# Optimization experiments

Measured on AMD Instinct MI355X. Metric: run time of the kernel, lower is better.

The kernel has to match this reference:

```python
import jax, jax.numpy as jnp
import numpy as np

EPS = 1e-8

def _normalize(a):
    return a / jnp.clip(jnp.linalg.norm(a, axis=-1, keepdims=True), EPS)

def _cosine(a, b):
    # pairwise cosine similarity: [Na, d] x [Nb, d] -> [Na, Nb]
    return _normalize(a) @ _normalize(b).T

def setup_inputs() -> dict:
    key = jax.random.key(0)
    n, k, q, d = 100, 5, 75, 4096
    x = jax.random.normal(key, (n * (k + q), d), dtype=jnp.float32)
    tao = jnp.full((1,), 10.0, dtype=jnp.float32)
    return {"x": x, "tao": tao, "n": n, "k": k, "q": q}

def reference(x, tao, n, k, q):
    d = x.shape[-1]
    x = x.reshape(n, k + q, d)
    support = x[:, :k]                      # [n, k, d]
    query = x[:, k:].reshape(n * q, d)      # [NQ, d]
    NQ = n * q
    proto = support.mean(axis=1)            # [n, d]

    pre_sim = _cosine(query, proto)         # [NQ, n]
    pre_label = jnp.argmax(pre_sim, axis=1) # [NQ]

    # vectorized per-class masked softmax aggregation (replaces Python loop)
    cls_ids = jnp.arange(n)
    mask = pre_label[None, :] == cls_ids[:, None]            # [n, NQ]
    logits_q = jnp.where(mask, pre_sim.T, -jnp.inf)          # [n, NQ]
    proto_n = _normalize(proto)
    self_sim = jnp.sum(proto_n * proto_n, axis=-1)           # [n], cosine(proto, proto)
    logits = jnp.concatenate([logits_q, self_sim[:, None]], axis=1)  # [n, NQ+1]
    w = jax.nn.softmax(logits, axis=1)                       # [n, NQ+1]
    adapted_proto = w[:, :NQ] @ query + w[:, NQ:] * proto    # [n, d]

    sim = _cosine(query, adapted_proto)                      # [NQ, n]
    return tao.reshape(()) * sim
```

## Files before the change

### kernel.cpp

```cpp
#include <hip/hip_runtime.h>
#include <hip/hip_bf16.h>
#include <math.h>

#define NQUERY 7500
#define NCLS   100
#define DIM    4096
#define KQ     75
#define KSUP   5
#define RPC    80
#define MPAD   7552
#define NPAD   112
#define CAPQ   256
#define RCAP   2048
#define EPSF   1e-8f
#define SELEM  845824
#define SLICE_BYTES 3383296u

typedef __attribute__((ext_vector_type(8))) short bf16x8;
typedef __attribute__((ext_vector_type(4))) float f32x4;

__device__ __forceinline__ int xrow_of_query(int j) {
    return (j / KQ) * RPC + KSUP + (j % KQ);
}
__device__ __forceinline__ short bf16t(float x) {
    union { float f; unsigned u; } v; v.f = x;
    return (short)(v.u >> 16);
}
__device__ __forceinline__ float bf16hi(float x) {
    union { float f; unsigned u; } v; v.f = x;
    v.u &= 0xFFFF0000u; return v.f;
}
__device__ __forceinline__ void gload_lds16(const short* g, short* l) {
    __builtin_amdgcn_global_load_lds(
        (const __attribute__((address_space(1))) unsigned int*)g,
        (__attribute__((address_space(3))) unsigned int*)l, 16, 0, 0);
}

__global__ __launch_bounds__(256) void k_proto1(const float* __restrict__ x,
        float* __restrict__ proto, float* __restrict__ norm2) {
    const int c = blockIdx.x, ch = blockIdx.y, t = threadIdx.x;
    const int i = ch * 1024 + t * 4;
    const float* b0 = x + (size_t)(c * RPC) * DIM;
    f32x4 s = {0.f, 0.f, 0.f, 0.f};
#pragma unroll
    for (int r = 0; r < KSUP; ++r)
        s += *(const f32x4*)(b0 + (size_t)r * DIM + i);
    s = s / 5.0f;
    *(f32x4*)(proto + (size_t)c*DIM + i) = s;
    float ssq = s[0]*s[0] + s[1]*s[1] + s[2]*s[2] + s[3]*s[3];
    for (int o = 32; o; o >>= 1) ssq += __shfl_down(ssq, o);
    if ((t & 63) == 0) atomicAdd(&norm2[c], ssq);
}

__global__ __launch_bounds__(256) void k_proto2(const float* __restrict__ proto,
        const float* __restrict__ norm2, short* __restrict__ Phi, short* __restrict__ Plo,
        float* __restrict__ es) {
    const int c = blockIdx.x, t = threadIdx.x;
    const int nt = c >> 4, lm = c & 15;
    if (c >= NCLS) {
        for (int g = t; g < 512; g += 256) {
            const int kstep = g >> 2, kq = g & 3;
            size_t o = (((size_t)(nt * 128 + kstep) * 4 + kq) * 16 + lm) * 8;
            bf16x8 z = {0,0,0,0,0,0,0,0};
            *(bf16x8*)(Phi + o) = z;
            *(bf16x8*)(Plo + o) = z;
        }
        return;
    }
    const float tot = norm2[c];
    const float inv = 1.f / fmaxf(sqrtf(tot), EPSF);
    if (t == 0) es[c] = expf(tot * inv * inv);
    for (int g = t; g < 512; g += 256) {
        const int kstep = g >> 2, kq = g & 3;
        const float* src = proto + (size_t)c * DIM + kstep * 32 + kq * 8;
        f32x4 a = *(const f32x4*)src, b = *(const f32x4*)(src + 4);
        float fv[8] = {a[0],a[1],a[2],a[3],b[0],b[1],b[2],b[3]};
        bf16x8 h, l;
#pragma unroll
        for (int e = 0; e < 8; ++e) {
            float pn = fv[e] * inv;
            float hh = bf16hi(pn);
            h[e] = bf16t(pn);
            l[e] = bf16t(pn - hh);
        }
        size_t o = (((size_t)(nt * 128 + kstep) * 4 + kq) * 16 + lm) * 8;
        *(bf16x8*)(Phi + o) = h;
        *(bf16x8*)(Plo + o) = l;
    }
}

template<int TNKS>
__global__ __launch_bounds__(256) void k_gemm1(const float* __restrict__ x,
        const short* __restrict__ Phi, const short* __restrict__ Plo,
        float* __restrict__ Spart, float* __restrict__ nq2) {
    constexpr int KST = 128 / TNKS;
    constexpr int NG  = KST / 2;
    __shared__ short bbuf[28 * 512];
    const int bx = blockIdx.x, kz = blockIdx.y;
    const int w = threadIdx.x >> 6, lane = threadIdx.x & 63;
    const int lm = lane & 15, kq = lane >> 4;
    const int mt = bx * 4 + w;
    const int j = mt * 16 + lm;
    const int jc = j < NQUERY ? j : NQUERY - 1;
    const float* pa = x + (size_t)xrow_of_query(jc) * DIM + kq * 8;
    const int ks0 = kz * KST;

    f32x4 acc[7];
#pragma unroll
    for (int nt = 0; nt < 7; ++nt) acc[nt] = (f32x4){0.f,0.f,0.f,0.f};
    float ssq = 0.f;

    for (int g = 0; g < NG; ++g) {
        const int gk = ks0 + g * 2;
#pragma unroll
        for (int p = 0; p < 7; ++p) {
            const int cid = w * 7 + p;
            const int s = cid / 14, r = cid % 14, nt = r >> 1, hl = r & 1;
            const short* gsrc = (hl ? Plo : Phi) + ((size_t)(nt * 128 + gk + s) << 9);
            gload_lds16(gsrc + lane * 8, &bbuf[(cid << 9) + lane * 8]);
        }
        __syncthreads();
#pragma unroll
        for (int s = 0; s < 2; ++s) {
            const float* pas = pa + (gk + s) * 32;
            f32x4 f0 = *(const f32x4*)(pas);
            f32x4 f1 = *(const f32x4*)(pas + 4);
            float fv[8] = {f0[0],f0[1],f0[2],f0[3],f1[0],f1[1],f1[2],f1[3]};
            bf16x8 ah, al;
#pragma unroll
            for (int e = 0; e < 8; ++e) {
                float xx = fv[e];
                ssq += xx * xx;
                float hh = bf16hi(xx);
                ah[e] = bf16t(xx);
                al[e] = bf16t(xx - hh);
            }
#pragma unroll
            for (int nt = 0; nt < 7; ++nt) {
                const bf16x8 bh = *(const bf16x8*)(&bbuf[((s*14 + nt*2 + 0) << 9) + lane * 8]);
                const bf16x8 bl = *(const bf16x8*)(&bbuf[((s*14 + nt*2 + 1) << 9) + lane * 8]);
                acc[nt] = __builtin_amdgcn_mfma_f32_16x16x32_bf16(ah, bh, acc[nt], 0, 0, 0);
                acc[nt] = __builtin_amdgcn_mfma_f32_16x16x32_bf16(ah, bl, acc[nt], 0, 0, 0);
                acc[nt] = __builtin_amdgcn_mfma_f32_16x16x32_bf16(al, bh, acc[nt], 0, 0, 0);
            }
        }
        __syncthreads();
    }
    float s2 = ssq;
    s2 += __shfl_xor(s2, 16);
    s2 += __shfl_xor(s2, 32);
    if (kq == 0 && j < NQUERY) atomicAdd(&nq2[j], s2);

    float* sp = Spart + (size_t)kz * SELEM + (size_t)(mt * 16) * NPAD;
#pragma unroll
    for (int nt = 0; nt < 7; ++nt)
#pragma unroll
        for (int r = 0; r < 4; ++r)
            sp[(size_t)(kq * 4 + r) * NPAD + nt * 16 + lm] = acc[nt][r];
}

__global__ __launch_bounds__(256) void k_reduce1(const float* __restrict__ Spart,
        float* __restrict__ Sred, int nks) {
    const int idx = blockIdx.x * 256 + threadIdx.x;
    const size_t e = (size_t)idx * 4;
    f32x4 s = {0.f, 0.f, 0.f, 0.f};
    for (int kz = 0; kz < nks; ++kz)
        s += *(const f32x4*)(Spart + (size_t)kz * SELEM + e);
    *(f32x4*)(Sred + e) = s;
}

__global__ __launch_bounds__(256) void k_argmax(const float* __restrict__ S,
        const float* __restrict__ nq2, int* __restrict__ label, float* __restrict__ coef,
        float* __restrict__ invq, int* __restrict__ rcnt, int* __restrict__ rlist) {
    const int j = blockIdx.x * 256 + threadIdx.x;
    if (j >= NQUERY) return;
    const float* row = S + (size_t)j * NPAD;
    float m1 = -1e30f, m2 = -1e30f;
    int i1 = 0, i2 = 0;
    for (int c = 0; c < NCLS; ++c) {
        float v = row[c];
        if (v > m1) { m2 = m1; i2 = i1; m1 = v; i1 = c; }
        else if (v > m2) { m2 = v; i2 = c; }
    }
    const float inv = 1.f / fmaxf(sqrtf(nq2[j]), EPSF);
    invq[j] = inv;
    label[j] = i1;
    coef[j] = expf(m1 * inv);
    if ((m1 - m2) * inv < 1e-4f) {
        int p = atomicAdd(rcnt, 1);
        if (p < RCAP) rlist[p] = j | (i1 << 13) | (i2 << 20);
    }
}

__global__ __launch_bounds__(64) void k_refine(const float* __restrict__ x,
        const float* __restrict__ S, const float* __restrict__ invq,
        int* __restrict__ label, float* __restrict__ coef,
        const int* __restrict__ rcnt, const int* __restrict__ rlist) {
    const int cnt = min(*rcnt, RCAP);
    const int lane = threadIdx.x;
    for (int e = blockIdx.x; e < cnt; e += gridDim.x) {
        const int pk = rlist[e];
        const int j = pk & 8191, c1 = (pk >> 13) & 127, c2 = (pk >> 20) & 127;
        const float* xq = x + (size_t)xrow_of_query(j) * DIM;
        const int cc[2] = {c1, c2};
        double cosv[2];
#pragma unroll
        for (int s = 0; s < 2; ++s) {
            const float* xb = x + (size_t)(cc[s] * RPC) * DIM;
            double dt = 0.0, pp = 0.0, q2 = 0.0;
            for (int i = lane; i < DIM; i += 64) {
                double p = (double)xb[i] + (double)xb[i + DIM] + (double)xb[i + 2*DIM]
                         + (double)xb[i + 3*DIM] + (double)xb[i + 4*DIM];
                double qv = (double)xq[i];
                dt += p * qv; pp += p * p; q2 += qv * qv;
            }
            for (int o = 32; o; o >>= 1) {
                dt += __shfl_down(dt, o);
                pp += __shfl_down(pp, o);
                q2 += __shfl_down(q2, o);
            }
            cosv[s] = dt / (sqrt(pp) * sqrt(q2));
        }
        if (lane == 0) {
            int win = (cosv[1] > cosv[0] || (cosv[1] == cosv[0] && c2 < c1)) ? c2 : c1;
            if (win != c1) {
                label[j] = win;
                coef[j] = expf(S[(size_t)j * NPAD + win] * invq[j]);
            }
        }
    }
}

__global__ __launch_bounds__(256) void k_lists(const int* __restrict__ label,
        int* __restrict__ cls_cnt, int* __restrict__ cls_list) {
    const int j = blockIdx.x * 256 + threadIdx.x;
    if (j >= NQUERY) return;
    const int c = label[j];
    const int p = atomicAdd(&cls_cnt[c], 1);
    if (p < CAPQ) cls_list[c * CAPQ + p] = j;
}

__global__ __launch_bounds__(128) void k_adapt(const float* __restrict__ x,
        const float* __restrict__ coef, const int* __restrict__ cls_cnt,
        const int* __restrict__ cls_list, float* __restrict__ APpart) {
    const int cx = blockIdx.x, c = blockIdx.y, sl = blockIdx.z;
    const int i0 = cx * 512 + threadIdx.x * 4;
    const int n = min(cls_cnt[c], CAPQ);
    f32x4 acc = {0.f, 0.f, 0.f, 0.f};
    for (int e = sl; e < n; e += 4) {
        const int j = cls_list[c * CAPQ + e];
        const float cf = coef[j];
        const f32x4 v = *(const f32x4*)(x + (size_t)xrow_of_query(j) * DIM + i0);
        acc += v * cf;
    }
    *(f32x4*)(APpart + (size_t)sl * NCLS * DIM + (size_t)c * DIM + i0) = acc;
}

__global__ __launch_bounds__(256) void k_ap1(float* __restrict__ APpart,
        const float* __restrict__ proto, const float* __restrict__ es,
        float* __restrict__ norm2b) {
    const int c = blockIdx.x, ch = blockIdx.y, t = threadIdx.x;
    const int i = ch * 1024 + t * 4;
    const float e = es[c];
    f32x4 s = {0.f, 0.f, 0.f, 0.f};
#pragma unroll
    for (int sl = 0; sl < 4; ++sl)
        s += *(const f32x4*)(APpart + (size_t)sl * NCLS * DIM + (size_t)c * DIM + i);
    f32x4 pr = *(const f32x4*)(proto + (size_t)c*DIM + i);
    s += pr * e;
    *(f32x4*)(APpart + (size_t)c*DIM + i) = s;
    float ssq = s[0]*s[0] + s[1]*s[1] + s[2]*s[2] + s[3]*s[3];
    for (int o = 32; o; o >>= 1) ssq += __shfl_down(ssq, o);
    if ((t & 63) == 0) atomicAdd(&norm2b[c], ssq);
}

__global__ __launch_bounds__(256) void k_ap2(const float* __restrict__ AP0,
        const float* __restrict__ norm2b, short* __restrict__ APhi) {
    const int c = blockIdx.x, t = threadIdx.x;
    const int nt = c >> 4, lm = c & 15;
    if (c >= NCLS) {
        for (int g = t; g < 512; g += 256) {
            const int kstep = g >> 2, kq = g & 3;
            size_t o = (((size_t)(nt * 128 + kstep) * 4 + kq) * 16 + lm) * 8;
            bf16x8 z = {0,0,0,0,0,0,0,0};
            *(bf16x8*)(APhi + o) = z;
        }
        return;
    }
    const float inv = 1.f / fmaxf(sqrtf(norm2b[c]), EPSF);
    for (int g = t; g < 512; g += 256) {
        const int kstep = g >> 2, kq = g & 3;
        const float* src = AP0 + (size_t)c * DIM + kstep * 32 + kq * 8;
        f32x4 a = *(const f32x4*)src, b = *(const f32x4*)(src + 4);
        float fv[8] = {a[0],a[1],a[2],a[3],b[0],b[1],b[2],b[3]};
        bf16x8 h;
#pragma unroll
        for (int e = 0; e < 8; ++e) h[e] = bf16t(fv[e] * inv);
        size_t o = (((size_t)(nt * 128 + kstep) * 4 + kq) * 16 + lm) * 8;
        *(bf16x8*)(APhi + o) = h;
    }
}

template<int TNKS>
__global__ __launch_bounds__(256) void k_gemm2(const float* __restrict__ x,
        const short* __restrict__ APhi, float* __restrict__ Opart) {
    constexpr int KST = 128 / TNKS;
    constexpr int NG  = KST / 2;
    __shared__ short bbuf[14 * 512];
    const int bx = blockIdx.x, kz = blockIdx.y;
    const int w = threadIdx.x >> 6, lane = threadIdx.x & 63;
    const int lm = lane & 15, kq = lane >> 4;
    const int mt = bx * 4 + w;
    const int j = mt * 16 + lm;
    const int jc = j < NQUERY ? j : NQUERY - 1;
    const float* pa = x + (size_t)xrow_of_query(jc) * DIM + kq * 8;
    const int ks0 = kz * KST;

    f32x4 acc[7];
#pragma unroll
    for (int nt = 0; nt < 7; ++nt) acc[nt] = (f32x4){0.f,0.f,0.f,0.f};

    for (int g = 0; g < NG; ++g) {
        const int gk = ks0 + g * 2;
#pragma unroll
        for (int p = 0; p < 4; ++p) {
            const int cid = w * 4 + p;
            if (cid < 14) {
                const int s = cid / 7, nt = cid % 7;
                const short* gsrc = APhi + ((size_t)(nt * 128 + gk + s) << 9);
                gload_lds16(gsrc + lane * 8, &bbuf[(cid << 9) + lane * 8]);
            }
        }
        __syncthreads();
#pragma unroll
        for (int s = 0; s < 2; ++s) {
            const float* pas = pa + (gk + s) * 32;
            f32x4 f0 = *(const f32x4*)(pas);
            f32x4 f1 = *(const f32x4*)(pas + 4);
            float fv[8] = {f0[0],f0[1],f0[2],f0[3],f1[0],f1[1],f1[2],f1[3]};
            bf16x8 ah;
#pragma unroll
            for (int e = 0; e < 8; ++e) ah[e] = bf16t(fv[e]);
#pragma unroll
            for (int nt = 0; nt < 7; ++nt) {
                const bf16x8 bh = *(const bf16x8*)(&bbuf[((s*7 + nt) << 9) + lane * 8]);
                acc[nt] = __builtin_amdgcn_mfma_f32_16x16x32_bf16(ah, bh, acc[nt], 0, 0, 0);
            }
        }
        __syncthreads();
    }
    float* op = Opart + (size_t)kz * SELEM + (size_t)(mt * 16) * NPAD;
#pragma unroll
    for (int nt = 0; nt < 7; ++nt)
#pragma unroll
        for (int r = 0; r < 4; ++r)
            op[(size_t)(kq * 4 + r) * NPAD + nt * 16 + lm] = acc[nt][r];
}

__global__ __launch_bounds__(256) void k_reduce2(const float* __restrict__ Opart,
        const float* __restrict__ invq, const float* __restrict__ tao,
        float* __restrict__ out, int nks) {
    const int idx = blockIdx.x * 256 + threadIdx.x;
    if (idx >= NQUERY * 25) return;
    const int j = idx / 25, c4 = (idx % 25) * 4;
    const size_t e = (size_t)j * NPAD + c4;
    f32x4 s = {0.f, 0.f, 0.f, 0.f};
    for (int kz = 0; kz < nks; ++kz)
        s += *(const f32x4*)(Opart + (size_t)kz * SELEM + e);
    const float sc = tao[0] * invq[j];
    *(f32x4*)(out + (size_t)j * NCLS + c4) = s * sc;
}

#define OFF_RCNT   0u
#define OFF_CCNT   256u
#define OFF_N2     768u
#define OFF_N2B    1280u
#define OFF_NQ2    1792u
#define ZERO_BYTES 32768u
#define OFF_ES     32768u
#define OFF_INVQ   33280u
#define OFF_LABEL  63488u
#define OFF_COEF   93696u
#define OFF_RLIST  123904u
#define OFF_CLIST  132096u
#define OFF_PROTO  234496u
#define OFF_PHI    1872896u
#define OFF_PLO    2790400u
#define OFF_APHI   3707904u
#define OFF_SRED   4625408u
#define OFF_APPART 8008704u
#define OFF_PART   14562304u

extern "C" void kernel_launch(void* const* d_in, const int* in_sizes, int n_in,
                              void* d_out, int out_size, void* d_ws, size_t ws_size,
                              hipStream_t stream) {
    const float* x   = (const float*)d_in[0];
    const float* tao = (const float*)d_in[1];
    char* ws = (char*)d_ws;

    int*   rcnt    = (int*)  (ws + OFF_RCNT);
    int*   ccnt    = (int*)  (ws + OFF_CCNT);
    float* norm2   = (float*)(ws + OFF_N2);
    float* norm2b  = (float*)(ws + OFF_N2B);
    float* nq2     = (float*)(ws + OFF_NQ2);
    float* es      = (float*)(ws + OFF_ES);
    float* invq    = (float*)(ws + OFF_INVQ);
    int*   label   = (int*)  (ws + OFF_LABEL);
    float* coef    = (float*)(ws + OFF_COEF);
    int*   rlist   = (int*)  (ws + OFF_RLIST);
    int*   clist   = (int*)  (ws + OFF_CLIST);
    float* proto   = (float*)(ws + OFF_PROTO);
    short* Phi     = (short*)(ws + OFF_PHI);
    short* Plo     = (short*)(ws + OFF_PLO);
    short* APhi    = (short*)(ws + OFF_APHI);
    float* Sred    = (float*)(ws + OFF_SRED);
    float* APpart  = (float*)(ws + OFF_APPART);
    float* Part    = (float*)(ws + OFF_PART);

    int nks = 1;
    if (ws_size > (size_t)OFF_PART + SLICE_BYTES) {
        size_t avail = (ws_size - OFF_PART) / SLICE_BYTES;
        nks = avail >= 8 ? 8 : (int)avail;
        while (nks & (nks - 1)) nks &= nks - 1;
    }

    hipMemsetAsync(ws, 0, ZERO_BYTES, stream);

    k_proto1 <<<dim3(NCLS, 4), 256, 0, stream>>>(x, proto, norm2);
    k_proto2 <<<NPAD, 256, 0, stream>>>(proto, norm2, Phi, Plo, es);

    switch (nks) {
        case 8:  k_gemm1<8> <<<dim3(118, 8), 256, 0, stream>>>(x, Phi, Plo, Part, nq2); break;
        case 4:  k_gemm1<4> <<<dim3(118, 4), 256, 0, stream>>>(x, Phi, Plo, Part, nq2); break;
        case 2:  k_gemm1<2> <<<dim3(118, 2), 256, 0, stream>>>(x, Phi, Plo, Part, nq2); break;
        default: k_gemm1<1> <<<dim3(118, 1), 256, 0, stream>>>(x, Phi, Plo, Part, nq2); break;
    }
    k_reduce1<<<826, 256, 0, stream>>>(Part, Sred, nks);
    k_argmax <<<30, 256, 0, stream>>>(Sred, nq2, label, coef, invq, rcnt, rlist);
    k_refine <<<512, 64, 0, stream>>>(x, Sred, invq, label, coef, rcnt, rlist);
    k_lists  <<<30, 256, 0, stream>>>(label, ccnt, clist);
    k_adapt  <<<dim3(8, NCLS, 4), 128, 0, stream>>>(x, coef, ccnt, clist, APpart);
    k_ap1    <<<dim3(NCLS, 4), 256, 0, stream>>>(APpart, proto, es, norm2b);
    k_ap2    <<<NPAD, 256, 0, stream>>>(APpart, norm2b, APhi);
    switch (nks) {
        case 8:  k_gemm2<8> <<<dim3(118, 8), 256, 0, stream>>>(x, APhi, Part); break;
        case 4:  k_gemm2<4> <<<dim3(118, 4), 256, 0, stream>>>(x, APhi, Part); break;
        case 2:  k_gemm2<2> <<<dim3(118, 2), 256, 0, stream>>>(x, APhi, Part); break;
        default: k_gemm2<1> <<<dim3(118, 1), 256, 0, stream>>>(x, APhi, Part); break;
    }
    k_reduce2<<<733, 256, 0, stream>>>(Part, invq, tao, (float*)d_out, nks);
}
```

Baseline: 360.5 us.

## Fuse prototype and adapted-prototype norm kernels; allow 16-way K split

Merges k_proto1/k_proto2 into one kernel per class that computes the mean, the norm via a block reduction, and the bf16 hi/lo tiles. It also merges k_ap1/k_ap2 into k_apnorm the same way, which removes two launches and the global atomics. The K-split cap for both GEMMs rises from 8 to 16 when workspace allows, giving more blocks in flight at the cost of more partial sums to reduce. The fused kernels use only 100 blocks, so each one has more serial work.

```diff
diff --git a/kernel.cpp b/kernel.cpp
--- a/kernel.cpp
+++ b/kernel.cpp
@@ -17,6 +17,7 @@
 #define SLICE_BYTES 3383296u
 
 typedef __attribute__((ext_vector_type(8))) short bf16x8;
+typedef __attribute__((ext_vector_type(4))) short s16x4;
 typedef __attribute__((ext_vector_type(4))) float f32x4;
 
 __device__ __forceinline__ int xrow_of_query(int j) {
@@ -36,24 +37,12 @@
         (__attribute__((address_space(3))) unsigned int*)l, 16, 0, 0);
 }
 
-__global__ __launch_bounds__(256) void k_proto1(const float* __restrict__ x,
-        float* __restrict__ proto, float* __restrict__ norm2) {
-    const int c = blockIdx.x, ch = blockIdx.y, t = threadIdx.x;
-    const int i = ch * 1024 + t * 4;
-    const float* b0 = x + (size_t)(c * RPC) * DIM;
-    f32x4 s = {0.f, 0.f, 0.f, 0.f};
-#pragma unroll
-    for (int r = 0; r < KSUP; ++r)
-        s += *(const f32x4*)(b0 + (size_t)r * DIM + i);
-    s = s / 5.0f;
-    *(f32x4*)(proto + (size_t)c*DIM + i) = s;
-    float ssq = s[0]*s[0] + s[1]*s[1] + s[2]*s[2] + s[3]*s[3];
-    for (int o = 32; o; o >>= 1) ssq += __shfl_down(ssq, o);
-    if ((t & 63) == 0) atomicAdd(&norm2[c], ssq);
-}
-
-__global__ __launch_bounds__(256) void k_proto2(const float* __restrict__ proto,
-        const float* __restrict__ norm2, short* __restrict__ Phi, short* __restrict__ Plo,
+__device__ __forceinline__ size_t tile_off(int nt, int lm, int i) {
+    return (((size_t)(nt * 128 + (i >> 5)) * 4 + ((i >> 3) & 3)) * 16 + lm) * 8 + (i & 7);
+}
+
+__global__ __launch_bounds__(256) void k_proto(const float* __restrict__ x,
+        float* __restrict__ proto, short* __restrict__ Phi, short* __restrict__ Plo,
         float* __restrict__ es) {
     const int c = blockIdx.x, t = threadIdx.x;
     const int nt = c >> 4, lm = c & 15;
@@ -65,27 +54,51 @@
             *(bf16x8*)(Phi + o) = z;
             *(bf16x8*)(Plo + o) = z;
         }
+        if (t == 0) es[c] = 0.f;
         return;
     }
-    const float tot = norm2[c];
-    const float inv = 1.f / fmaxf(sqrtf(tot), EPSF);
-    if (t == 0) es[c] = expf(tot * inv * inv);
-    for (int g = t; g < 512; g += 256) {
-        const int kstep = g >> 2, kq = g & 3;
-        const float* src = proto + (size_t)c * DIM + kstep * 32 + kq * 8;
-        f32x4 a = *(const f32x4*)src, b = *(const f32x4*)(src + 4);
-        float fv[8] = {a[0],a[1],a[2],a[3],b[0],b[1],b[2],b[3]};
-        bf16x8 h, l;
-#pragma unroll
-        for (int e = 0; e < 8; ++e) {
-            float pn = fv[e] * inv;
+    __shared__ float red[4];
+    __shared__ float s_inv;
+    const float* b0 = x + (size_t)(c * RPC) * DIM;
+    float v[16];
+    float ssq = 0.f;
+#pragma unroll
+    for (int p = 0; p < 4; ++p) {
+        const int i = p * 1024 + t * 4;
+        f32x4 s = {0.f, 0.f, 0.f, 0.f};
+#pragma unroll
+        for (int r = 0; r < KSUP; ++r)
+            s += *(const f32x4*)(b0 + (size_t)r * DIM + i);
+        s = s / 5.0f;
+        *(f32x4*)&v[p*4] = s;
+        *(f32x4*)(proto + (size_t)c*DIM + i) = s;
+        ssq += s[0]*s[0] + s[1]*s[1] + s[2]*s[2] + s[3]*s[3];
+    }
+    for (int o = 32; o; o >>= 1) ssq += __shfl_down(ssq, o);
+    if ((t & 63) == 0) red[t >> 6] = ssq;
+    __syncthreads();
+    if (t == 0) {
+        float tot = red[0] + red[1] + red[2] + red[3];
+        float inv = 1.f / fmaxf(sqrtf(tot), EPSF);
+        s_inv = inv;
+        es[c] = expf(tot * inv * inv);
+    }
+    __syncthreads();
+    const float inv = s_inv;
+#pragma unroll
+    for (int p = 0; p < 4; ++p) {
+        const int i = p * 1024 + t * 4;
+        s16x4 h, l;
+#pragma unroll
+        for (int e = 0; e < 4; ++e) {
+            float pn = v[p*4+e] * inv;
             float hh = bf16hi(pn);
             h[e] = bf16t(pn);
             l[e] = bf16t(pn - hh);
         }
-        size_t o = (((size_t)(nt * 128 + kstep) * 4 + kq) * 16 + lm) * 8;
-        *(bf16x8*)(Phi + o) = h;
-        *(bf16x8*)(Plo + o) = l;
+        const size_t o = tile_off(nt, lm, i);
+        *(s16x4*)(Phi + o) = h;
+        *(s16x4*)(Plo + o) = l;
     }
 }
 
@@ -256,26 +269,9 @@
     *(f32x4*)(APpart + (size_t)sl * NCLS * DIM + (size_t)c * DIM + i0) = acc;
 }
 
-__global__ __launch_bounds__(256) void k_ap1(float* __restrict__ APpart,
+__global__ __launch_bounds__(256) void k_apnorm(const float* __restrict__ APpart,
         const float* __restrict__ proto, const float* __restrict__ es,
-        float* __restrict__ norm2b) {
-    const int c = blockIdx.x, ch = blockIdx.y, t = threadIdx.x;
-    const int i = ch * 1024 + t * 4;
-    const float e = es[c];
-    f32x4 s = {0.f, 0.f, 0.f, 0.f};
-#pragma unroll
-    for (int sl = 0; sl < 4; ++sl)
-        s += *(const f32x4*)(APpart + (size_t)sl * NCLS * DIM + (size_t)c * DIM + i);
-    f32x4 pr = *(const f32x4*)(proto + (size_t)c*DIM + i);
-    s += pr * e;
-    *(f32x4*)(APpart + (size_t)c*DIM + i) = s;
-    float ssq = s[0]*s[0] + s[1]*s[1] + s[2]*s[2] + s[3]*s[3];
-    for (int o = 32; o; o >>= 1) ssq += __shfl_down(ssq, o);
-    if ((t & 63) == 0) atomicAdd(&norm2b[c], ssq);
-}
-
-__global__ __launch_bounds__(256) void k_ap2(const float* __restrict__ AP0,
-        const float* __restrict__ norm2b, short* __restrict__ APhi) {
+        short* __restrict__ APhi) {
     const int c = blockIdx.x, t = threadIdx.x;
     const int nt = c >> 4, lm = c & 15;
     if (c >= NCLS) {
@@ -287,17 +283,39 @@
         }
         return;
     }
-    const float inv = 1.f / fmaxf(sqrtf(norm2b[c]), EPSF);
-    for (int g = t; g < 512; g += 256) {
-        const int kstep = g >> 2, kq = g & 3;
-        const float* src = AP0 + (size_t)c * DIM + kstep * 32 + kq * 8;
-        f32x4 a = *(const f32x4*)src, b = *(const f32x4*)(src + 4);
-        float fv[8] = {a[0],a[1],a[2],a[3],b[0],b[1],b[2],b[3]};
-        bf16x8 h;
-#pragma unroll
-        for (int e = 0; e < 8; ++e) h[e] = bf16t(fv[e] * inv);
-        size_t o = (((size_t)(nt * 128 + kstep) * 4 + kq) * 16 + lm) * 8;
-        *(bf16x8*)(APhi + o) = h;
+    __shared__ float red[4];
+    __shared__ float s_inv;
+    const float e0 = es[c];
+    float v[16];
+    float ssq = 0.f;
+#pragma unroll
+    for (int p = 0; p < 4; ++p) {
+        const int i = p * 1024 + t * 4;
+        f32x4 s = {0.f, 0.f, 0.f, 0.f};
+#pragma unroll
+        for (int sl = 0; sl < 4; ++sl)
+            s += *(const f32x4*)(APpart + (size_t)sl * NCLS * DIM + (size_t)c * DIM + i);
+        f32x4 pr = *(const f32x4*)(proto + (size_t)c*DIM + i);
+        s += pr * e0;
+        *(f32x4*)&v[p*4] = s;
+        ssq += s[0]*s[0] + s[1]*s[1] + s[2]*s[2] + s[3]*s[3];
+    }
+    for (int o = 32; o; o >>= 1) ssq += __shfl_down(ssq, o);
+    if ((t & 63) == 0) red[t >> 6] = ssq;
+    __syncthreads();
+    if (t == 0) {
+        float tot = red[0] + red[1] + red[2] + red[3];
+        s_inv = 1.f / fmaxf(sqrtf(tot), EPSF);
+    }
+    __syncthreads();
+    const float inv = s_inv;
+#pragma unroll
+    for (int p = 0; p < 4; ++p) {
+        const int i = p * 1024 + t * 4;
+        s16x4 h;
+#pragma unroll
+        for (int e = 0; e < 4; ++e) h[e] = bf16t(v[p*4+e] * inv);
+        *(s16x4*)(APhi + tile_off(nt, lm, i)) = h;
     }
 }
 
@@ -373,8 +391,6 @@
 
 #define OFF_RCNT   0u
 #define OFF_CCNT   256u
-#define OFF_N2     768u
-#define OFF_N2B    1280u
 #define OFF_NQ2    1792u
 #define ZERO_BYTES 32768u
 #define OFF_ES     32768u
@@ -400,8 +416,6 @@
 
     int*   rcnt    = (int*)  (ws + OFF_RCNT);
     int*   ccnt    = (int*)  (ws + OFF_CCNT);
-    float* norm2   = (float*)(ws + OFF_N2);
-    float* norm2b  = (float*)(ws + OFF_N2B);
     float* nq2     = (float*)(ws + OFF_NQ2);
     float* es      = (float*)(ws + OFF_ES);
     float* invq    = (float*)(ws + OFF_INVQ);
@@ -420,33 +434,32 @@
     int nks = 1;
     if (ws_size > (size_t)OFF_PART + SLICE_BYTES) {
         size_t avail = (ws_size - OFF_PART) / SLICE_BYTES;
-        nks = avail >= 8 ? 8 : (int)avail;
+        nks = avail >= 16 ? 16 : (int)avail;
         while (nks & (nks - 1)) nks &= nks - 1;
     }
 
     hipMemsetAsync(ws, 0, ZERO_BYTES, stream);
 
-    k_proto1 <<<dim3(NCLS, 4), 256, 0, stream>>>(x, proto, norm2);
-    k_proto2 <<<NPAD, 256, 0, stream>>>(proto, norm2, Phi, Plo, es);
-
+    k_proto <<<NPAD, 256, 0, stream>>>(x, proto, Phi, Plo, es);
     switch (nks) {
-        case 8:  k_gemm1<8> <<<dim3(118, 8), 256, 0, stream>>>(x, Phi, Plo, Part, nq2); break;
-        case 4:  k_gemm1<4> <<<dim3(118, 4), 256, 0, stream>>>(x, Phi, Plo, Part, nq2); break;
-        case 2:  k_gemm1<2> <<<dim3(118, 2), 256, 0, stream>>>(x, Phi, Plo, Part, nq2); break;
-        default: k_gemm1<1> <<<dim3(118, 1), 256, 0, stream>>>(x, Phi, Plo, Part, nq2); break;
+        case 16: k_gemm1<16><<<dim3(118, 16), 256, 0, stream>>>(x, Phi, Plo, Part, nq2); break;
+        case 8:  k_gemm1<8> <<<dim3(118, 8),  256, 0, stream>>>(x, Phi, Plo, Part, nq2); break;
+        case 4:  k_gemm1<4> <<<dim3(118, 4),  256, 0, stream>>>(x, Phi, Plo, Part, nq2); break;
+        case 2:  k_gemm1<2> <<<dim3(118, 2),  256, 0, stream>>>(x, Phi, Plo, Part, nq2); break;
+        default: k_gemm1<1> <<<dim3(118, 1),  256, 0, stream>>>(x, Phi, Plo, Part, nq2); break;
     }
     k_reduce1<<<826, 256, 0, stream>>>(Part, Sred, nks);
     k_argmax <<<30, 256, 0, stream>>>(Sred, nq2, label, coef, invq, rcnt, rlist);
     k_refine <<<512, 64, 0, stream>>>(x, Sred, invq, label, coef, rcnt, rlist);
     k_lists  <<<30, 256, 0, stream>>>(label, ccnt, clist);
     k_adapt  <<<dim3(8, NCLS, 4), 128, 0, stream>>>(x, coef, ccnt, clist, APpart);
-    k_ap1    <<<dim3(NCLS, 4), 256, 0, stream>>>(APpart, proto, es, norm2b);
-    k_ap2    <<<NPAD, 256, 0, stream>>>(APpart, norm2b, APhi);
+    k_apnorm <<<NPAD, 256, 0, stream>>>(APpart, proto, es, APhi);
     switch (nks) {
-        case 8:  k_gemm2<8> <<<dim3(118, 8), 256, 0, stream>>>(x, APhi, Part); break;
-        case 4:  k_gemm2<4> <<<dim3(118, 4), 256, 0, stream>>>(x, APhi, Part); break;
-        case 2:  k_gemm2<2> <<<dim3(118, 2), 256, 0, stream>>>(x, APhi, Part); break;
-        default: k_gemm2<1> <<<dim3(118, 1), 256, 0, stream>>>(x, APhi, Part); break;
+        case 16: k_gemm2<16><<<dim3(118, 16), 256, 0, stream>>>(x, APhi, Part); break;
+        case 8:  k_gemm2<8> <<<dim3(118, 8),  256, 0, stream>>>(x, APhi, Part); break;
+        case 4:  k_gemm2<4> <<<dim3(118, 4),  256, 0, stream>>>(x, APhi, Part); break;
+        case 2:  k_gemm2<2> <<<dim3(118, 2),  256, 0, stream>>>(x, APhi, Part); break;
+        default: k_gemm2<1> <<<dim3(118, 1),  256, 0, stream>>>(x, APhi, Part); break;
     }
     k_reduce2<<<733, 256, 0, stream>>>(Part, invq, tao, (float*)d_out, nks);
 }
```

Measured after the change: 365.1 us. Within noise of the previous version (+1.3%).
